# Optimization experiments

Measured on AMD Instinct MI355X. Metric: run time of the kernel, lower is better.

## Reference

```python
import jax, jax.numpy as jnp
import numpy as np

IN_DIM = 4096
OUT_DIM = 4096
BLOCK = 256
RANK = 16
B_IN = IN_DIM // BLOCK   # 16
B_OUT = OUT_DIM // BLOCK # 16


def setup_inputs() -> dict:
    key = jax.random.key(0)
    k1, k2, k3, k4, k5 = jax.random.split(key, 5)
    x = jax.random.normal(k1, (2, 1024, IN_DIM), dtype=jnp.float32)
    # S ~ U[0, 2)
    S = jax.random.uniform(k2, (B_OUT, B_IN, RANK), dtype=jnp.float32, minval=0.0, maxval=2.0)
    std = np.sqrt(0.02).astype(np.float32)
    U = jax.random.normal(k3, (B_OUT, RANK, BLOCK), dtype=jnp.float32) * std
    Vt = jax.random.normal(k4, (B_IN, BLOCK, RANK), dtype=jnp.float32) * std
    # kaiming_uniform_ on a (1, out_dim) tensor with default a=sqrt(5): bound = 1/sqrt(fan_in) = 1/sqrt(out_dim)
    bound = float(1.0 / np.sqrt(OUT_DIM))
    bias = jax.random.uniform(k5, (OUT_DIM,), dtype=jnp.float32, minval=-bound, maxval=bound)
    return {"x": x, "S": S, "U": U, "Vt": Vt, "bias": bias}


def reference(x, S, U, Vt, bias):
    # Faithful to Blast.forward: it reconstructs the dense weight by running
    # forward2 on an identity matrix (which ALSO adds bias to every row of W),
    # then computes addmm(bias, x, W).
    # Block (i_in, i_out) of W0 = Vt[i_in] @ diag(S[i_out, i_in]) @ U[i_out].
    W0 = jnp.einsum('ipr,oir,orq->ipoq', Vt, S, U).reshape(IN_DIM, OUT_DIM)
    W = W0 + bias[None, :]  # identity-trick: forward2(I) adds bias to each of the in_dim rows
    out = x @ W + bias      # [B, S, out_dim]
    return out
```

## Files before the change

kernel.cpp:

```cpp
#include <hip/hip_runtime.h>

#define IN_DIM  4096
#define OUT_DIM 4096
#define RANK    16
#define NBLK    16
#define KDIM    256

typedef __attribute__((ext_vector_type(8))) __bf16 bf16x8;
typedef __attribute__((ext_vector_type(4))) __bf16 bf16x4;
typedef __attribute__((ext_vector_type(4))) float  f32x4;


__device__ __forceinline__ void split_bf16(float v, __bf16& h, __bf16& l) {
    h = (__bf16)v;
    l = (__bf16)(v - (float)h);
}

__global__ __launch_bounds__(256) void build_packs(const float* __restrict__ S,
                                                   const float* __restrict__ U,
                                                   const float* __restrict__ Vt,
                                                   bf16x8* __restrict__ Bhi,
                                                   bf16x8* __restrict__ Blo,
                                                   bf16x8* __restrict__ Vhi,
                                                   bf16x8* __restrict__ Vlo) {
    const int blk = blockIdx.x;
    if (blk < 512) {
        int t  = blk * 256 + threadIdx.x;
        int c  = t & 15;
        int ko = (t >> 4) & 31;
        int nt = t >> 9;
        int o  = nt >> 4;
        int i  = ko >> 1;
        int q  = ((nt & 15) << 4) | c;
        int r0 = (ko & 1) << 3;
        const float* Sp = S + ((o * NBLK + i) * RANK + r0);
        const float* Up = U + (size_t)o * RANK * 256 + q;
        bf16x8 hi, lo;
#pragma unroll
        for (int j = 0; j < 8; ++j) {
            float w = Sp[j] * Up[(size_t)(r0 + j) * 256];
            __bf16 h, l;
            split_bf16(w, h, l);
            hi[j] = h; lo[j] = l;
        }
        Bhi[t] = hi;
        Blo[t] = lo;
    } else {
        int t  = (blk - 512) * 256 + threadIdx.x;
        int c  = t & 15;
        int p0 = (t >> 4) << 3;
        int i  = t >> 9;
        int pbase = (p0 & 255);
        const float* vp = Vt + ((size_t)(i * 256 + pbase)) * RANK + c;
        bf16x8 hi, lo;
#pragma unroll
        for (int j = 0; j < 8; ++j) {
            float w = vp[(size_t)j * RANK];
            __bf16 h, l;
            split_bf16(w, h, l);
            hi[j] = h; lo[j] = l;
        }
        Vhi[t] = hi;
        Vlo[t] = lo;
    }
}

__global__ __launch_bounds__(256) void factor_mfma(const float* __restrict__ x,
                                                   const bf16x8* __restrict__ Vhi,
                                                   const bf16x8* __restrict__ Vlo,
                                                   bf16x4* __restrict__ Ahi4,
                                                   bf16x4* __restrict__ Alo4,
                                                   float* __restrict__ rowsum_p,
                                                   int M) {
    const int tid = threadIdx.x;
    const int l   = tid & 63;
    const int w   = tid >> 6;
    const int job = blockIdx.x * 4 + w;
    const int i   = job & 15;
    const int mt  = job >> 4;
    const int row = l & 15;
    const int qt  = l >> 4;

    const float* xp = x + (size_t)(mt * 16 + row) * IN_DIM + i * 256 + qt * 8;

    f32x4 acc = {0.f, 0.f, 0.f, 0.f};
    float rs = 0.f;
#pragma unroll
    for (int ks = 0; ks < 8; ++ks) {
        float4 a = *reinterpret_cast<const float4*>(xp + ks * 32);
        float4 b = *reinterpret_cast<const float4*>(xp + ks * 32 + 4);
        rs += (a.x + a.y) + (a.z + a.w) + (b.x + b.y) + (b.z + b.w);
        float vv[8] = {a.x, a.y, a.z, a.w, b.x, b.y, b.z, b.w};
        bf16x8 xh, xl;
#pragma unroll
        for (int jj = 0; jj < 8; ++jj) {
            __bf16 h, lo_;
            split_bf16(vv[jj], h, lo_);
            xh[jj] = h; xl[jj] = lo_;
        }
        size_t vidx = (size_t)((i * 8 + ks) * 4 + qt) * 16 + row;
        bf16x8 vh = Vhi[vidx];
        bf16x8 vl = Vlo[vidx];
        acc = __builtin_amdgcn_mfma_f32_16x16x32_bf16(vh, xh, acc, 0, 0, 0);
        acc = __builtin_amdgcn_mfma_f32_16x16x32_bf16(vh, xl, acc, 0, 0, 0);
        acc = __builtin_amdgcn_mfma_f32_16x16x32_bf16(vl, xh, acc, 0, 0, 0);
    }

    rs += __shfl_xor(rs, 16, 64);
    rs += __shfl_xor(rs, 32, 64);
    if (l < 16)
        rowsum_p[(size_t)i * M + mt * 16 + l] = rs;

    bf16x4 hi, lo;
#pragma unroll
    for (int reg = 0; reg < 4; ++reg) {
        __bf16 h, lo_;
        split_bf16(acc[reg], h, lo_);
        hi[reg] = h; lo[reg] = lo_;
    }
    size_t o4 = ((size_t)(mt * 32 + i * 2 + (l >> 5)) * 16 + row) * 2 + ((l >> 4) & 1);
    Ahi4[o4] = hi;
    Alo4[o4] = lo;
}

__global__ __launch_bounds__(256) void apply_mfma(const bf16x8* __restrict__ Ahi,
                                                  const bf16x8* __restrict__ Alo,
                                                  const bf16x8* __restrict__ Bhi,
                                                  const bf16x8* __restrict__ Blo,
                                                  const float* __restrict__ rowsum_p,
                                                  const float* __restrict__ bias,
                                                  float* __restrict__ out, int M) {
    const int mblocks = M >> 6;
    const int nb  = blockIdx.x;
    const int q   = gridDim.x >> 3;
    const int lg  = (nb & 7) * q + (nb >> 3);
    const int mr  = lg % mblocks;
    const int nc  = lg / mblocks;
    const int m0  = mr * 64, n0 = nc * 256;

    const int tid = threadIdx.x;
    const int l   = tid & 63;
    const int wid = __builtin_amdgcn_readfirstlane(tid >> 6);
    const int wm  = wid & 1, wn = wid >> 1;
    const int kq  = l >> 4, c = l & 15;

    __shared__ float rstot_s[64];
    if (tid < 64) {
        float s = 1.0f;
#pragma unroll
        for (int i = 0; i < NBLK; ++i) s += rowsum_p[(size_t)i * M + m0 + tid];
        rstot_s[tid] = s;
    }
    __syncthreads();

    f32x4 acc[2][8];
#pragma unroll
    for (int f = 0; f < 2; ++f)
#pragma unroll
        for (int nf = 0; nf < 8; ++nf) acc[f][nf] = f32x4{0.f, 0.f, 0.f, 0.f};

    const int mtb = (m0 >> 4) + wm * 2;
    const int ntb = nc * 16 + wn * 8;

#pragma unroll 2
    for (int s = 0; s < 8; ++s) {
        const int kb = 4 * s + kq;
        bf16x8 ah[2], al[2];
#pragma unroll
        for (int f = 0; f < 2; ++f) {
            size_t off = (size_t)((mtb + f) * 32 + kb) * 16 + c;
            ah[f] = Ahi[off];
            al[f] = Alo[off];
        }
#pragma unroll
        for (int nf = 0; nf < 8; ++nf) {
            size_t off = (size_t)((ntb + nf) * 32 + kb) * 16 + c;
            bf16x8 bh = Bhi[off];
            bf16x8 bl = Blo[off];
#pragma unroll
            for (int f = 0; f < 2; ++f) {
                acc[f][nf] = __builtin_amdgcn_mfma_f32_16x16x32_bf16(ah[f], bh, acc[f][nf], 0, 0, 0);
                acc[f][nf] = __builtin_amdgcn_mfma_f32_16x16x32_bf16(ah[f], bl, acc[f][nf], 0, 0, 0);
                acc[f][nf] = __builtin_amdgcn_mfma_f32_16x16x32_bf16(al[f], bh, acc[f][nf], 0, 0, 0);
            }
        }
    }

#pragma unroll
    for (int f = 0; f < 2; ++f) {
        const int rloc = wm * 32 + f * 16 + kq * 4;
        const int rowb = m0 + rloc;
        float rsv[4];
#pragma unroll
        for (int reg = 0; reg < 4; ++reg) rsv[reg] = rstot_s[rloc + reg];
#pragma unroll
        for (int nf = 0; nf < 8; ++nf) {
            const int n = n0 + wn * 128 + nf * 16 + c;
            const float bv = bias[n];
#pragma unroll
            for (int reg = 0; reg < 4; ++reg)
                out[(size_t)(rowb + reg) * OUT_DIM + n] = acc[f][nf][reg] + rsv[reg] * bv;
        }
    }
}

extern "C" void kernel_launch(void* const* d_in, const int* in_sizes, int n_in,
                              void* d_out, int out_size, void* d_ws, size_t ws_size,
                              hipStream_t stream) {
    const float* x    = (const float*)d_in[0];
    const float* S    = (const float*)d_in[1];
    const float* U    = (const float*)d_in[2];
    const float* Vt   = (const float*)d_in[3];
    const float* bias = (const float*)d_in[4];
    float* out = (float*)d_out;
    const int M = in_sizes[0] / IN_DIM;

    char* ws = (char*)d_ws;
    bf16x8* Bhi     = (bf16x8*)ws;
    bf16x8* Blo     = (bf16x8*)(ws + (2u << 20));
    bf16x8* Ahi     = (bf16x8*)(ws + (4u << 20));
    bf16x8* Alo     = (bf16x8*)(ws + (5u << 20));
    bf16x8* Vhi     = (bf16x8*)(ws + (6u << 20));
    bf16x8* Vlo     = (bf16x8*)(ws + (6u << 20) + (128u << 10));
    float* rowsum_p = (float*)(ws + (6u << 20) + (256u << 10));

    build_packs<<<544, 256, 0, stream>>>(S, U, Vt, Bhi, Blo, Vhi, Vlo);
    factor_mfma<<<M / 4, 256, 0, stream>>>(x, Vhi, Vlo,
                                           (bf16x4*)Ahi, (bf16x4*)Alo, rowsum_p, M);
    apply_mfma<<<(M / 64) * (OUT_DIM / 256), 256, 0, stream>>>(
        Ahi, Alo, Bhi, Blo, rowsum_p, bias, out, M);
}
```

Before: 114.0 us.

## Double-buffer apply operands in LDS via async global_load_lds and shrink N tile

The apply kernel now stages A and B hi/lo fragments into a double-buffered LDS area using global_load_lds, prefetching the next K step while MFMAs run on the current one. The N tile is halved from 256 to 128 columns, which doubles the grid and cuts accumulator registers, and launch bounds request 3 blocks per CU. This targets global-load latency stalls and low occupancy. In exchange it adds a barrier every K step, and the M-block count is hardcoded to 32, which assumes M equals 2048.

After: 116.9 us. 1.03x slower.

```diff
diff --git a/kernel.cpp b/kernel.cpp
--- a/kernel.cpp
+++ b/kernel.cpp
@@ -123,60 +123,80 @@
     Alo4[o4] = lo;
 }
 
-__global__ __launch_bounds__(256) void apply_mfma(const bf16x8* __restrict__ Ahi,
-                                                  const bf16x8* __restrict__ Alo,
-                                                  const bf16x8* __restrict__ Bhi,
-                                                  const bf16x8* __restrict__ Blo,
-                                                  const float* __restrict__ rowsum_p,
-                                                  const float* __restrict__ bias,
-                                                  float* __restrict__ out, int M) {
-    const int mblocks = M >> 6;
+__global__ __launch_bounds__(256, 3) void apply_mfma(const bf16x8* __restrict__ Ahi,
+                                                     const bf16x8* __restrict__ Alo,
+                                                     const bf16x8* __restrict__ Bhi,
+                                                     const bf16x8* __restrict__ Blo,
+                                                     const float* __restrict__ rowsum_p,
+                                                     const float* __restrict__ bias,
+                                                     float* __restrict__ out, int M) {
+    __shared__ bf16x8 smem[2][1536];
+    __shared__ float rstot_s[64];
+
     const int nb  = blockIdx.x;
     const int q   = gridDim.x >> 3;
     const int lg  = (nb & 7) * q + (nb >> 3);
-    const int mr  = lg % mblocks;
-    const int nc  = lg / mblocks;
-    const int m0  = mr * 64, n0 = nc * 256;
+    const int mr  = lg & 31;
+    const int nc  = lg >> 5;
+    const int m0  = mr * 64, n0 = nc * 128;
+    const int mtb0 = m0 >> 4;
+    const int ntb0 = n0 >> 4;
 
     const int tid = threadIdx.x;
     const int l   = tid & 63;
-    const int wid = __builtin_amdgcn_readfirstlane(tid >> 6);
-    const int wm  = wid & 1, wn = wid >> 1;
+    const int w   = __builtin_amdgcn_readfirstlane(tid >> 6);
+    const int wm  = w & 1, wn = w >> 1;
     const int kq  = l >> 4, c = l & 15;
 
-    __shared__ float rstot_s[64];
+#define STAGE(s_, buf_)                                                              \
+    {                                                                                \
+        _Pragma("unroll")                                                            \
+        for (int j = 0; j < 6; ++j) {                                                \
+            const int sl = w * 6 + j;                                                \
+            const bf16x8* gbase;                                                     \
+            if (sl < 8) {                                                            \
+                gbase = ((sl >> 2) ? Alo : Ahi)                                      \
+                      + ((size_t)(mtb0 + (sl & 3)) * 32 + 4 * (s_)) * 16;            \
+            } else {                                                                 \
+                const int b = sl - 8;                                                \
+                gbase = ((b >> 3) ? Blo : Bhi)                                       \
+                      + ((size_t)(ntb0 + (b & 7)) * 32 + 4 * (s_)) * 16;             \
+            }                                                                        \
+            __builtin_amdgcn_global_load_lds(                                        \
+                (const __attribute__((address_space(1))) unsigned*)(gbase + l),      \
+                (__attribute__((address_space(3))) unsigned*)&smem[buf_][sl * 64],   \
+                16, 0, 0);                                                           \
+        }                                                                            \
+    }
+
+    f32x4 acc[2][4];
+#pragma unroll
+    for (int f = 0; f < 2; ++f)
+#pragma unroll
+        for (int nf = 0; nf < 4; ++nf) acc[f][nf] = f32x4{0.f, 0.f, 0.f, 0.f};
+
+    STAGE(0, 0);
     if (tid < 64) {
-        float s = 1.0f;
-#pragma unroll
-        for (int i = 0; i < NBLK; ++i) s += rowsum_p[(size_t)i * M + m0 + tid];
-        rstot_s[tid] = s;
+        float ssum = 1.0f;
+#pragma unroll
+        for (int i = 0; i < NBLK; ++i) ssum += rowsum_p[(size_t)i * M + m0 + tid];
+        rstot_s[tid] = ssum;
     }
     __syncthreads();
 
-    f32x4 acc[2][8];
-#pragma unroll
-    for (int f = 0; f < 2; ++f)
-#pragma unroll
-        for (int nf = 0; nf < 8; ++nf) acc[f][nf] = f32x4{0.f, 0.f, 0.f, 0.f};
-
-    const int mtb = (m0 >> 4) + wm * 2;
-    const int ntb = nc * 16 + wn * 8;
-
-#pragma unroll 2
     for (int s = 0; s < 8; ++s) {
-        const int kb = 4 * s + kq;
+        if (s < 7) STAGE(s + 1, (s + 1) & 1);
+        const bf16x8* sb = smem[s & 1];
         bf16x8 ah[2], al[2];
 #pragma unroll
         for (int f = 0; f < 2; ++f) {
-            size_t off = (size_t)((mtb + f) * 32 + kb) * 16 + c;
-            ah[f] = Ahi[off];
-            al[f] = Alo[off];
-        }
-#pragma unroll
-        for (int nf = 0; nf < 8; ++nf) {
-            size_t off = (size_t)((ntb + nf) * 32 + kb) * 16 + c;
-            bf16x8 bh = Bhi[off];
-            bf16x8 bl = Blo[off];
+            ah[f] = sb[(wm * 2 + f) * 64 + l];
+            al[f] = sb[(4 + wm * 2 + f) * 64 + l];
+        }
+#pragma unroll
+        for (int nf = 0; nf < 4; ++nf) {
+            bf16x8 bh = sb[512 + (wn * 4 + nf) * 64 + l];
+            bf16x8 bl = sb[1024 + (wn * 4 + nf) * 64 + l];
 #pragma unroll
             for (int f = 0; f < 2; ++f) {
                 acc[f][nf] = __builtin_amdgcn_mfma_f32_16x16x32_bf16(ah[f], bh, acc[f][nf], 0, 0, 0);
@@ -184,7 +204,9 @@
                 acc[f][nf] = __builtin_amdgcn_mfma_f32_16x16x32_bf16(al[f], bh, acc[f][nf], 0, 0, 0);
             }
         }
-    }
+        __syncthreads();
+    }
+#undef STAGE
 
 #pragma unroll
     for (int f = 0; f < 2; ++f) {
@@ -194,8 +216,8 @@
 #pragma unroll
         for (int reg = 0; reg < 4; ++reg) rsv[reg] = rstot_s[rloc + reg];
 #pragma unroll
-        for (int nf = 0; nf < 8; ++nf) {
-            const int n = n0 + wn * 128 + nf * 16 + c;
+        for (int nf = 0; nf < 4; ++nf) {
+            const int n = n0 + wn * 64 + nf * 16 + c;
             const float bv = bias[n];
 #pragma unroll
             for (int reg = 0; reg < 4; ++reg)
@@ -227,6 +249,6 @@
     build_packs<<<544, 256, 0, stream>>>(S, U, Vt, Bhi, Blo, Vhi, Vlo);
     factor_mfma<<<M / 4, 256, 0, stream>>>(x, Vhi, Vlo,
                                            (bf16x4*)Ahi, (bf16x4*)Alo, rowsum_p, M);
-    apply_mfma<<<(M / 64) * (OUT_DIM / 256), 256, 0, stream>>>(
+    apply_mfma<<<(M / 64) * (OUT_DIM / 128), 256, 0, stream>>>(
         Ahi, Alo, Bhi, Blo, rowsum_p, bias, out, M);
 }
```
